# Kernel optimization log

Hardware: AMD Instinct MI355X
Metric: run time of the kernel (lower is better)

The kernel has to match this reference:

```python
import jax, jax.numpy as jnp
import numpy as np
from jax import lax

# LRN hyperparameters (from module __init__)
K = 2.0
KERNEL = 5
ALPHA = 1e-4
BETA = 0.75
PAD = KERNEL // 2


def setup_inputs() -> dict:
    key = jax.random.key(0)
    x = jax.random.normal(key, (16, 96, 224, 224), dtype=jnp.float32)
    return {"x": x}


def reference(x) -> jnp.ndarray:
    # Spatial local response norm: per-channel k x k box sum of squares
    # (equivalent to Unfold(kernel, pad=kernel//2) -> view -> square -> sum over window).
    sq = x * x
    ssq = lax.reduce_window(
        sq,
        jnp.float32(0.0),
        lax.add,
        window_dimensions=(1, 1, KERNEL, KERNEL),
        window_strides=(1, 1, 1, 1),
        padding=((0, 0), (0, 0), (PAD, PAD), (PAD, PAD)),
    )
    denom = (K + ALPHA * ssq) ** BETA
    return x / denom
```

## Files before the change

### kernel.cpp

```cpp
#include <hip/hip_runtime.h>


typedef float f4 __attribute__((ext_vector_type(4)));

#define LRN_H 224
#define LRN_W 224
#define LRN_WQ 56
#define LRN_R 2
#define LRN_IN (LRN_R + 4)
#define LRN_SLABS (LRN_H / LRN_R)
#define LRN_PLANE (LRN_H * LRN_W)
#define LRN_BLOCKS 43008
#define LRN_BPX (LRN_BLOCKS / 8)

__global__ __launch_bounds__(256, 7) void LocalResponseNorm_17420387352942_kernel(
        const float* __restrict__ x, float* __restrict__ out) {
    const int b    = blockIdx.x;
    const int swz  = (b & 7) * LRN_BPX + (b >> 3);
    const int q    = threadIdx.x & 63;
    const int wave = threadIdx.x >> 6;
    const int job  = swz * 4 + wave;
    const int plane = job / LRN_SLABS;
    const int slab  = job - plane * LRN_SLABS;
    const int h0    = slab * LRN_R;

    const int qe = min(q, LRN_WQ - 1);
    const float* __restrict__ px = x   + (size_t)plane * LRN_PLANE + (qe << 2);
    float* __restrict__       po = out + (size_t)plane * LRN_PLANE + (qe << 2);

    const float mL = (qe > 0)          ? 1.0f : 0.0f;
    const float mR = (qe < LRN_WQ - 1) ? 1.0f : 0.0f;
    const int offL = (qe > 0)          ? -4 : 0;
    const int offR = (qe < LRN_WQ - 1) ?  4 : 0;
    const bool wr  = (q < LRN_WQ);

    f4 xc[LRN_IN];
#pragma unroll
    for (int r = 0; r < LRN_IN; ++r) {
        const int row = h0 + r - 2;
        const int rc  = min(max(row, 0), LRN_H - 1);
        xc[r] = *(const f4*)(px + rc * LRN_W);
    }

    f4 acc0 = (f4){0.f, 0.f, 0.f, 0.f};
    f4 acc1 = (f4){0.f, 0.f, 0.f, 0.f};

#pragma unroll
    for (int r = 0; r < LRN_IN; ++r) {
        const int row = h0 + r - 2;
        const float mV = (row >= 0 && row < LRN_H) ? 1.0f : 0.0f;
        const int rc   = min(max(row, 0), LRN_H - 1);
        const float* rp = px + rc * LRN_W;
        f4 xl = *(const f4*)(rp + offL);
        f4 xr = *(const f4*)(rp + offR);

        float a  = xl[2] * xl[2] * mL;
        float bb = xl[3] * xl[3] * mL;
        float c0 = xc[r][0] * xc[r][0];
        float c1 = xc[r][1] * xc[r][1];
        float c2 = xc[r][2] * xc[r][2];
        float c3 = xc[r][3] * xc[r][3];
        float d0 = xr[0] * xr[0] * mR;
        float d1 = xr[1] * xr[1] * mR;
        float t  = c1 + c2;
        f4 rs;
        rs[0] = (a + bb + c0 + t) * mV;
        rs[1] = (bb + c0 + t + c3) * mV;
        rs[2] = (c0 + t + c3 + d0) * mV;
        rs[3] = (t + c3 + d0 + d1) * mV;

        if (r <= 4) acc0 += rs;
        if (r >= 1) acc1 += rs;
    }

    f4 o0, o1;
#pragma unroll
    for (int j = 0; j < 4; ++j) {
        float d0  = fmaf(1e-4f, acc0[j], 2.0f);
        float rs0 = __builtin_amdgcn_rsqf(d0);
        o0[j] = xc[2][j] * rs0 * __builtin_amdgcn_sqrtf(rs0);
        float d1  = fmaf(1e-4f, acc1[j], 2.0f);
        float rs1 = __builtin_amdgcn_rsqf(d1);
        o1[j] = xc[3][j] * rs1 * __builtin_amdgcn_sqrtf(rs1);
    }
    if (wr) {
        __builtin_nontemporal_store(o0, (f4*)(po + h0 * LRN_W));
        __builtin_nontemporal_store(o1, (f4*)(po + (h0 + 1) * LRN_W));
    }
}

extern "C" void kernel_launch(void* const* d_in, const int* in_sizes, int n_in,
                              void* d_out, int out_size, void* d_ws, size_t ws_size,
                              hipStream_t stream) {
    const float* x = (const float*)d_in[0];
    float* out = (float*)d_out;
    dim3 block(256, 1, 1);
    dim3 grid(LRN_BLOCKS, 1, 1);
    LocalResponseNorm_17420387352942_kernel<<<grid, block, 0, stream>>>(x, out);
}
```

Before: 559.7 us.

## Process eight output rows per wave with double-buffered neighbor loads

Each wave now computes eight output rows instead of two, so the four halo rows are loaded once per eight outputs rather than once per two. This cuts redundant global reads of center and neighbor columns. The grid shrinks accordingly and the occupancy hint drops from 7 to 4 to leave room for more registers. Left and right neighbor vectors are prefetched two rows ahead in a small double buffer so their loads overlap the arithmetic. The catch is fewer resident waves and higher register pressure.

```diff
diff --git a/kernel.cpp b/kernel.cpp
--- a/kernel.cpp
+++ b/kernel.cpp
@@ -6,14 +6,14 @@
 #define LRN_H 224
 #define LRN_W 224
 #define LRN_WQ 56
-#define LRN_R 2
+#define LRN_R 8
 #define LRN_IN (LRN_R + 4)
 #define LRN_SLABS (LRN_H / LRN_R)
 #define LRN_PLANE (LRN_H * LRN_W)
-#define LRN_BLOCKS 43008
+#define LRN_BLOCKS 10752
 #define LRN_BPX (LRN_BLOCKS / 8)
 
-__global__ __launch_bounds__(256, 7) void LocalResponseNorm_17420387352942_kernel(
+__global__ __launch_bounds__(256, 4) void LocalResponseNorm_17420387352942_kernel(
         const float* __restrict__ x, float* __restrict__ out) {
     const int b    = blockIdx.x;
     const int swz  = (b & 7) * LRN_BPX + (b >> 3);
@@ -37,22 +37,37 @@
     f4 xc[LRN_IN];
 #pragma unroll
     for (int r = 0; r < LRN_IN; ++r) {
-        const int row = h0 + r - 2;
-        const int rc  = min(max(row, 0), LRN_H - 1);
+        const int rc = min(max(h0 + r - 2, 0), LRN_H - 1);
         xc[r] = *(const f4*)(px + rc * LRN_W);
     }
 
-    f4 acc0 = (f4){0.f, 0.f, 0.f, 0.f};
-    f4 acc1 = (f4){0.f, 0.f, 0.f, 0.f};
+    f4 xlp[2], xrp[2];
+#pragma unroll
+    for (int r = 0; r < 2; ++r) {
+        const int rc = min(max(h0 + r - 2, 0), LRN_H - 1);
+        const float* rp = px + rc * LRN_W;
+        xlp[r] = *(const f4*)(rp + offL);
+        xrp[r] = *(const f4*)(rp + offR);
+    }
+
+    f4 acc[LRN_R];
+#pragma unroll
+    for (int i = 0; i < LRN_R; ++i) acc[i] = (f4){0.f, 0.f, 0.f, 0.f};
 
 #pragma unroll
     for (int r = 0; r < LRN_IN; ++r) {
+        f4 xl = xlp[r & 1];
+        f4 xr = xrp[r & 1];
+        if (r + 2 < LRN_IN) {
+            const int rc2 = min(max(h0 + r, 0), LRN_H - 1);
+            const float* rp2 = px + rc2 * LRN_W;
+            xlp[r & 1] = *(const f4*)(rp2 + offL);
+            xrp[r & 1] = *(const f4*)(rp2 + offR);
+        }
+
         const int row = h0 + r - 2;
-        const float mV = (row >= 0 && row < LRN_H) ? 1.0f : 0.0f;
-        const int rc   = min(max(row, 0), LRN_H - 1);
-        const float* rp = px + rc * LRN_W;
-        f4 xl = *(const f4*)(rp + offL);
-        f4 xr = *(const f4*)(rp + offR);
+        const float mV = (r >= 2 && r < 10) ? 1.0f
+                        : ((row >= 0 && row < LRN_H) ? 1.0f : 0.0f);
 
         float a  = xl[2] * xl[2] * mL;
         float bb = xl[3] * xl[3] * mL;
@@ -69,23 +84,22 @@
         rs[2] = (c0 + t + c3 + d0) * mV;
         rs[3] = (t + c3 + d0 + d1) * mV;
 
-        if (r <= 4) acc0 += rs;
-        if (r >= 1) acc1 += rs;
+#pragma unroll
+        for (int i = 0; i < LRN_R; ++i) {
+            if (i <= r && r <= i + 4) acc[i] += rs;
+        }
     }
 
-    f4 o0, o1;
 #pragma unroll
-    for (int j = 0; j < 4; ++j) {
-        float d0  = fmaf(1e-4f, acc0[j], 2.0f);
-        float rs0 = __builtin_amdgcn_rsqf(d0);
-        o0[j] = xc[2][j] * rs0 * __builtin_amdgcn_sqrtf(rs0);
-        float d1  = fmaf(1e-4f, acc1[j], 2.0f);
-        float rs1 = __builtin_amdgcn_rsqf(d1);
-        o1[j] = xc[3][j] * rs1 * __builtin_amdgcn_sqrtf(rs1);
-    }
-    if (wr) {
-        __builtin_nontemporal_store(o0, (f4*)(po + h0 * LRN_W));
-        __builtin_nontemporal_store(o1, (f4*)(po + (h0 + 1) * LRN_W));
+    for (int i = 0; i < LRN_R; ++i) {
+        f4 o;
+#pragma unroll
+        for (int j = 0; j < 4; ++j) {
+            float d   = fmaf(1e-4f, acc[i][j], 2.0f);
+            float rsq = __builtin_amdgcn_rsqf(d);
+            o[j] = xc[i + 2][j] * rsq * __builtin_amdgcn_sqrtf(rsq);
+        }
+        if (wr) __builtin_nontemporal_store(o, (f4*)(po + (h0 + i) * LRN_W));
     }
 }
 
```

New measurement: 519.4 us. -7.2%, faster.
